# Optimization experiments

Hardware: AMD Instinct MI355X
Metric: run time of the kernel (lower is better)

## Reference

```python
import jax, jax.numpy as jnp
import numpy as np

HEADS = 16
DIM_HEAD = 64
SCALE = DIM_HEAD ** -0.5
LN_EPS = 1e-5


def setup_inputs() -> dict:
    key = jax.random.key(0)
    k1, k2, k3 = jax.random.split(key, 3)
    b, s, d = 2, 2048, 1024
    inner = HEADS * DIM_HEAD
    x = jax.random.normal(k1, (b, s, d), dtype=jnp.float32)
    w_qkv = jax.random.normal(k2, (d, 3 * inner), dtype=jnp.float32) * (d ** -0.5)
    w_out = jax.random.normal(k3, (inner, d), dtype=jnp.float32) * (inner ** -0.5)
    return {
        "x": x,
        "ln_gamma": jnp.ones((d,), jnp.float32),
        "ln_beta": jnp.zeros((d,), jnp.float32),
        "w_qkv": w_qkv,
        "w_out": w_out,
        "b_out": jnp.zeros((d,), jnp.float32),
    }


def _layernorm(x, gamma, beta):
    mu = jnp.mean(x, axis=-1, keepdims=True)
    var = jnp.var(x, axis=-1, keepdims=True)
    return (x - mu) * jax.lax.rsqrt(var + LN_EPS) * gamma + beta


def reference(x, ln_gamma, ln_beta, w_qkv, w_out, b_out):
    b, s, d = x.shape
    xn = _layernorm(x, ln_gamma, ln_beta)
    qkv = xn @ w_qkv                       # [b, s, 3*inner]
    q, k, v = jnp.split(qkv, 3, axis=-1)
    def heads(t):
        return t.reshape(b, s, HEADS, DIM_HEAD).transpose(0, 2, 1, 3)  # [b, h, s, dh]
    q, k, v = heads(q), heads(k), heads(v)
    dots = jnp.einsum("bhqd,bhkd->bhqk", q, k) * SCALE   # [b, h, s, s]
    attn = jax.nn.softmax(dots, axis=-1)
    out = jnp.einsum("bhqk,bhkd->bhqd", attn, v)          # [b, h, s, dh]
    out = out.transpose(0, 2, 1, 3).reshape(b, s, HEADS * DIM_HEAD)
    return out @ w_out + b_out
```

## Files before the change

### kernel.cpp

```cpp
#include <hip/hip_runtime.h>
#include <hip/hip_bf16.h>
#include <stdint.h>

#define NH     16
#define DHEAD  64
#define SEQ    2048
#define DMODEL 1024
#define NBATCH 2
#define INNER  1024
#define QKVN   3072
#define ROWS   4096
#define ATT_QB 128
#define ATT_KB 64
#define KSPLIT 2

typedef __attribute__((ext_vector_type(8))) __bf16 bf16x8;
typedef __attribute__((ext_vector_type(4))) float floatx4;

__device__ __forceinline__ unsigned short f2bf(float f) {
    union { __bf16 b; unsigned short u; } c; c.b = (__bf16)f; return c.u;
}

typedef __attribute__((address_space(1))) void gvoid;
typedef __attribute__((address_space(3))) void lvoid;
__device__ __forceinline__ void gl_lds16(const void* g, void* l) {
    __builtin_amdgcn_global_load_lds((gvoid*)g, (lvoid*)l, 16, 0, 0);
}

__global__ __launch_bounds__(256) void transpose_f2b(
        const float* __restrict__ in, unsigned short* __restrict__ out,
        int rows, int cols) {
    __shared__ unsigned short tile[32][33];
    const int bx = blockIdx.x * 32, by = blockIdx.y * 32;
    const int tx = threadIdx.x & 31, ty = threadIdx.x >> 5;
    for (int i = ty; i < 32; i += 8)
        tile[i][tx] = f2bf(in[(size_t)(by + i) * cols + bx + tx]);
    __syncthreads();
    for (int i = ty; i < 32; i += 8)
        out[(size_t)(bx + i) * rows + by + tx] = tile[tx][i];
}

__global__ __launch_bounds__(256) void ln_kernel(
        const float* __restrict__ x,
        const float* __restrict__ gamma,
        const float* __restrict__ beta,
        unsigned short* __restrict__ xn) {
    __shared__ float red[4][2];
    const int row = blockIdx.x, t = threadIdx.x;
    const size_t base = (size_t)row * DMODEL + t * 4;
    float4 v = *(const float4*)(x + base);
    float s  = v.x + v.y + v.z + v.w;
    float ss = v.x*v.x + v.y*v.y + v.z*v.z + v.w*v.w;
    for (int off = 32; off >= 1; off >>= 1) {
        s  += __shfl_xor(s,  off);
        ss += __shfl_xor(ss, off);
    }
    const int w = t >> 6, lane = t & 63;
    if (lane == 0) { red[w][0] = s; red[w][1] = ss; }
    __syncthreads();
    if (t == 0) {
        float S  = red[0][0] + red[1][0] + red[2][0] + red[3][0];
        float SS = red[0][1] + red[1][1] + red[2][1] + red[3][1];
        float mu  = S * (1.f / DMODEL);
        float var = SS * (1.f / DMODEL) - mu * mu;
        red[0][0] = mu; red[0][1] = rsqrtf(var + 1e-5f);
    }
    __syncthreads();
    const float mu = red[0][0], rstd = red[0][1];
    float4 g = *(const float4*)(gamma + t * 4);
    float4 bb = *(const float4*)(beta + t * 4);
    ushort4 o;
    o.x = f2bf((v.x - mu) * rstd * g.x + bb.x);
    o.y = f2bf((v.y - mu) * rstd * g.y + bb.y);
    o.z = f2bf((v.z - mu) * rstd * g.z + bb.z);
    o.w = f2bf((v.w - mu) * rstd * g.w + bb.w);
    *(ushort4*)(xn + base) = o;
}

__global__ __launch_bounds__(256) void gemm_qkv(
        const unsigned short* __restrict__ A,
        const unsigned short* __restrict__ Bt,
        unsigned short* __restrict__ qP,
        unsigned short* __restrict__ kP,
        unsigned short* __restrict__ vT) {
    const int K = DMODEL;
    __shared__ __align__(16) unsigned short sA[128 * 32];
    __shared__ __align__(16) unsigned short sB[128 * 32];
    __shared__ __align__(16) unsigned short tb[2][64 * 72];
    const int t = threadIdx.x;
    const int mBase = blockIdx.y * 128, nBase = blockIdx.x * 128;
    const int w = t >> 6, lane = t & 63, quad = lane >> 4, l16 = lane & 15;
    const int wm = (w >> 1) * 64, wn = (w & 1) * 64;
    const int srow = t >> 2, sch = t & 3;
    floatx4 acc[4][4];
    for (int mi = 0; mi < 4; mi++)
        for (int ni = 0; ni < 4; ni++) acc[mi][ni] = (floatx4)0.f;

    for (int k0 = 0; k0 < K; k0 += 32) {
        #pragma unroll
        for (int c = 0; c < 2; c++) {
            const int row = c * 64 + srow;
            const int gcol = (sch ^ ((row >> 1) & 3)) * 8;
            gl_lds16(&A[(size_t)(mBase + row) * K + k0 + gcol], &sA[(c * 256 + w * 64) * 8]);
            gl_lds16(&Bt[(size_t)(nBase + row) * K + k0 + gcol], &sB[(c * 256 + w * 64) * 8]);
        }
        __syncthreads();
        bf16x8 af[4], bfv[4];
        #pragma unroll
        for (int mi = 0; mi < 4; mi++) {
            const int r = wm + mi * 16 + l16;
            af[mi] = *(const bf16x8*)&sA[r * 32 + (quad ^ ((r >> 1) & 3)) * 8];
        }
        #pragma unroll
        for (int ni = 0; ni < 4; ni++) {
            const int r = wn + ni * 16 + l16;
            bfv[ni] = *(const bf16x8*)&sB[r * 32 + (quad ^ ((r >> 1) & 3)) * 8];
        }
        #pragma unroll
        for (int mi = 0; mi < 4; mi++)
            #pragma unroll
            for (int ni = 0; ni < 4; ni++)
                acc[mi][ni] = __builtin_amdgcn_mfma_f32_16x16x32_bf16(
                    af[mi], bfv[ni], acc[mi][ni], 0, 0, 0);
        __syncthreads();
    }
    const int reg = nBase >> 10;
    if (reg == 2) {
        #pragma unroll
        for (int ni = 0; ni < 4; ni++) {
            const int col = nBase + wn + ni * 16 + l16;
            const int h = (col & 1023) >> 6, dh = col & 63;
            #pragma unroll
            for (int mi = 0; mi < 4; mi++) {
                const int row0 = mBase + wm + mi * 16 + quad * 4;
                const int b = row0 >> 11, s0 = row0 & 2047;
                ushort4 o;
                o.x = f2bf(acc[mi][ni][0]); o.y = f2bf(acc[mi][ni][1]);
                o.z = f2bf(acc[mi][ni][2]); o.w = f2bf(acc[mi][ni][3]);
                *(ushort4*)&vT[((size_t)(b * NH + h) * DHEAD + dh) * SEQ + s0] = o;
            }
        }
    } else {
        unsigned short* dst = (reg == 0) ? qP : kP;
        const float scl = (reg == 0) ? 0.125f : 1.f;
        const int hh = ((nBase + wn) & 1023) >> 6;
        #pragma unroll
        for (int ph = 0; ph < 2; ph++) {
            if ((w >> 1) == ph) {
                unsigned short* tb_ = &tb[w & 1][0];
                #pragma unroll
                for (int mi = 0; mi < 4; mi++)
                    #pragma unroll
                    for (int ni = 0; ni < 4; ni++)
                        #pragma unroll
                        for (int i = 0; i < 4; i++)
                            tb_[(mi * 16 + quad * 4 + i) * 72 + ni * 16 + l16] =
                                f2bf(acc[mi][ni][i] * scl);
                asm volatile("s_waitcnt lgkmcnt(0)" ::: "memory");
                const int row_g = mBase + wm + lane;
                const int b = row_g >> 11, sr = row_g & 2047;
                unsigned short* orow = dst + ((size_t)(b * NH + hh) * SEQ + sr) * DHEAD;
                #pragma unroll
                for (int c = 0; c < 8; c++)
                    *(bf16x8*)&orow[c * 8] = *(const bf16x8*)&tb_[lane * 72 + c * 8];
            }
            __syncthreads();
        }
    }
}

__global__ __launch_bounds__(256) void gemm_out(
        const unsigned short* __restrict__ A,
        const unsigned short* __restrict__ Bt,
        float* __restrict__ C,
        const int M, const int N, const int K,
        const float* __restrict__ bias) {
    __shared__ __align__(16) unsigned short sA[128 * 32];
    __shared__ __align__(16) unsigned short sB[64 * 32];
    const int t = threadIdx.x;
    const int mBase = blockIdx.y * 128, nBase = blockIdx.x * 64;
    const int w = t >> 6, lane = t & 63, quad = lane >> 4, l16 = lane & 15;
    const int wm = (w >> 1) * 64, wn = (w & 1) * 32;
    const int srow = t >> 2, sch = t & 3;
    floatx4 acc[4][2];
    for (int mi = 0; mi < 4; mi++)
        for (int ni = 0; ni < 2; ni++) acc[mi][ni] = (floatx4)0.f;

    for (int k0 = 0; k0 < K; k0 += 32) {
        #pragma unroll
        for (int c = 0; c < 2; c++) {
            const int row = c * 64 + srow;
            const int gcol = (sch ^ ((row >> 1) & 3)) * 8;
            gl_lds16(&A[(size_t)(mBase + row) * K + k0 + gcol], &sA[(c * 256 + w * 64) * 8]);
        }
        {
            const int gcol = (sch ^ ((srow >> 1) & 3)) * 8;
            gl_lds16(&Bt[(size_t)(nBase + srow) * K + k0 + gcol], &sB[(w * 64) * 8]);
        }
        __syncthreads();
        bf16x8 af[4], bfv[2];
        #pragma unroll
        for (int mi = 0; mi < 4; mi++) {
            const int r = wm + mi * 16 + l16;
            af[mi] = *(const bf16x8*)&sA[r * 32 + (quad ^ ((r >> 1) & 3)) * 8];
        }
        #pragma unroll
        for (int ni = 0; ni < 2; ni++) {
            const int r = wn + ni * 16 + l16;
            bfv[ni] = *(const bf16x8*)&sB[r * 32 + (quad ^ ((r >> 1) & 3)) * 8];
        }
        #pragma unroll
        for (int mi = 0; mi < 4; mi++)
            #pragma unroll
            for (int ni = 0; ni < 2; ni++)
                acc[mi][ni] = __builtin_amdgcn_mfma_f32_16x16x32_bf16(
                    af[mi], bfv[ni], acc[mi][ni], 0, 0, 0);
        __syncthreads();
    }
    #pragma unroll
    for (int mi = 0; mi < 4; mi++)
        #pragma unroll
        for (int ni = 0; ni < 2; ni++) {
            const int col = nBase + wn + ni * 16 + l16;
            const float badd = bias ? bias[col] : 0.f;
            #pragma unroll
            for (int i = 0; i < 4; i++) {
                const int row = mBase + wm + mi * 16 + quad * 4 + i;
                C[(size_t)row * N + col] = acc[mi][ni][i] + badd;
            }
        }
}

__global__ __launch_bounds__(256) void attn_kernel(
        const unsigned short* __restrict__ qP,
        const unsigned short* __restrict__ kP,
        const unsigned short* __restrict__ vT,
        float* __restrict__ Opart,
        float* __restrict__ lpart) {
    __shared__ __align__(16) unsigned short sK[2][ATT_KB * 64];
    __shared__ __align__(16) unsigned short sV[2][ATT_KB * 64];
    __shared__ __align__(16) unsigned short sP[4][2][16 * 64];
    const int t = threadIdx.x, w = t >> 6, lane = t & 63;
    const int quad = lane >> 4, l16 = lane & 15;
    const int bh = blockIdx.y, b = bh >> 4, h = bh & 15;
    const int z = blockIdx.z;
    const int kvBase = z * (SEQ / KSPLIT);
    const int qbase = blockIdx.x * ATT_QB + w * 32;
    const int swr = l16 & 7;

    bf16x8 aq[2][2];
    #pragma unroll
    for (int st = 0; st < 2; st++)
        #pragma unroll
        for (int hh = 0; hh < 2; hh++)
            aq[st][hh] = *(const bf16x8*)&qP[
                ((size_t)bh * SEQ + qbase + st * 16 + l16) * DHEAD + hh * 32 + quad * 8];

    floatx4 oac[2][4];
    float lS[2] = {0.f, 0.f};
    #pragma unroll
    for (int st = 0; st < 2; st++)
        #pragma unroll
        for (int c = 0; c < 4; c++) oac[st][c] = (floatx4)0.f;

    const unsigned short* kb = kP + (size_t)bh * SEQ * DHEAD;
    const unsigned short* vb = vT + (size_t)bh * DHEAD * SEQ;
    const int r8 = lane >> 3, sw8 = ((lane & 7) ^ r8) * 8;

    auto stage = [&](int it, int bi) {
        const int kv0 = kvBase + it * ATT_KB;
        #pragma unroll
        for (int ii = 0; ii < 2; ii++) {
            const int row = w * 16 + ii * 8 + r8;
            gl_lds16(kb + (size_t)(kv0 + row) * DHEAD + sw8,
                     (void*)&sK[bi][(w * 16 + ii * 8) * 64]);
            gl_lds16(vb + (size_t)row * SEQ + kv0 + sw8,
                     (void*)&sV[bi][(w * 16 + ii * 8) * 64]);
        }
    };
    stage(0, 0);

    const int NIT = SEQ / KSPLIT / ATT_KB;
    for (int it = 0; it < NIT; ++it) {
        __syncthreads();
        if (it + 1 < NIT) stage(it + 1, (it + 1) & 1);
        const unsigned short* sKb = &sK[it & 1][0];
        const unsigned short* sVb = &sV[it & 1][0];

        bf16x8 kf[4][2];
        #pragma unroll
        for (int c = 0; c < 4; c++)
            #pragma unroll
            for (int hh = 0; hh < 2; hh++)
                kf[c][hh] = *(const bf16x8*)&sKb[(c * 16 + l16) * 64 +
                                                 8 * (((hh << 2) | quad) ^ swr)];
        floatx4 sv[2][4];
        #pragma unroll
        for (int st = 0; st < 2; st++)
            #pragma unroll
            for (int c = 0; c < 4; c++) {
                floatx4 a = (floatx4)0.f;
                a = __builtin_amdgcn_mfma_f32_16x16x32_bf16(kf[c][0], aq[st][0], a, 0, 0, 0);
                a = __builtin_amdgcn_mfma_f32_16x16x32_bf16(kf[c][1], aq[st][1], a, 0, 0, 0);
                sv[st][c] = a;
            }
        #pragma unroll
        for (int st = 0; st < 2; st++) {
            float sum = 0.f;
            unsigned short* pb = (unsigned short*)&sP[w][st][0];
            #pragma unroll
            for (int c = 0; c < 4; c++) {
                float p0 = __expf(sv[st][c][0]), p1 = __expf(sv[st][c][1]);
                float p2 = __expf(sv[st][c][2]), p3 = __expf(sv[st][c][3]);
                sum += (p0 + p1) + (p2 + p3);
                ushort4 pk;
                pk.x = f2bf(p0); pk.y = f2bf(p1); pk.z = f2bf(p2); pk.w = f2bf(p3);
                *(ushort4*)&pb[l16 * 64 + 8 * ((((c << 1) | (quad >> 1))) ^ swr) + (quad & 1) * 4] = pk;
            }
            sum += __shfl_xor(sum, 16);
            sum += __shfl_xor(sum, 32);
            lS[st] += sum;
        }
        bf16x8 vf[4][2];
        #pragma unroll
        for (int c = 0; c < 4; c++)
            #pragma unroll
            for (int hh = 0; hh < 2; hh++)
                vf[c][hh] = *(const bf16x8*)&sVb[(c * 16 + l16) * 64 +
                                                 8 * (((hh << 2) | quad) ^ swr)];
        asm volatile("s_waitcnt lgkmcnt(0)" ::: "memory");
        #pragma unroll
        for (int st = 0; st < 2; st++) {
            const unsigned short* pb = (const unsigned short*)&sP[w][st][0];
            bf16x8 pf[2];
            #pragma unroll
            for (int hh = 0; hh < 2; hh++)
                pf[hh] = *(const bf16x8*)&pb[l16 * 64 + 8 * (((hh << 2) | quad) ^ swr)];
            #pragma unroll
            for (int c = 0; c < 4; c++) {
                oac[st][c] = __builtin_amdgcn_mfma_f32_16x16x32_bf16(vf[c][0], pf[0], oac[st][c], 0, 0, 0);
                oac[st][c] = __builtin_amdgcn_mfma_f32_16x16x32_bf16(vf[c][1], pf[1], oac[st][c], 0, 0, 0);
            }
        }
    }
    float* Ob = Opart + (size_t)z * ROWS * INNER;
    #pragma unroll
    for (int st = 0; st < 2; st++) {
        const size_t rb = (size_t)(b * SEQ + qbase + st * 16 + l16) * INNER + h * DHEAD;
        #pragma unroll
        for (int c = 0; c < 4; c++) {
            float4 o;
            o.x = oac[st][c][0]; o.y = oac[st][c][1];
            o.z = oac[st][c][2]; o.w = oac[st][c][3];
            *(float4*)&Ob[rb + c * 16 + quad * 4] = o;
        }
    }
    if (quad == 0) {
        #pragma unroll
        for (int st = 0; st < 2; st++)
            lpart[((size_t)z * NBATCH * NH + bh) * SEQ + qbase + st * 16 + l16] = lS[st];
    }
}

__global__ __launch_bounds__(256) void attn_combine(
        const float* __restrict__ Opart,
        const float* __restrict__ lpart,
        unsigned short* __restrict__ aout) {
    const int row = blockIdx.x, t = threadIdx.x;
    const int b = row >> 11, s = row & 2047;
    __shared__ float rls[16];
    if (t < 16) {
        const size_t i0 = ((size_t)(b * NH + t)) * SEQ + s;
        rls[t] = 1.f / (lpart[i0] + lpart[(size_t)NBATCH * NH * SEQ + i0]);
    }
    __syncthreads();
    const size_t base = (size_t)row * INNER + t * 4;
    float4 o0 = *(const float4*)(Opart + base);
    float4 o1 = *(const float4*)(Opart + (size_t)ROWS * INNER + base);
    const float rl = rls[t >> 4];
    ushort4 o;
    o.x = f2bf((o0.x + o1.x) * rl);
    o.y = f2bf((o0.y + o1.y) * rl);
    o.z = f2bf((o0.z + o1.z) * rl);
    o.w = f2bf((o0.w + o1.w) * rl);
    *(ushort4*)&aout[base] = o;
}

extern "C" void kernel_launch(void* const* d_in, const int* in_sizes, int n_in,
                              void* d_out, int out_size, void* d_ws, size_t ws_size,
                              hipStream_t stream) {
    const float* x     = (const float*)d_in[0];
    const float* gamma = (const float*)d_in[1];
    const float* beta  = (const float*)d_in[2];
    const float* wqkv  = (const float*)d_in[3];
    const float* wout  = (const float*)d_in[4];
    const float* bout  = (const float*)d_in[5];
    float* out = (float*)d_out;

    unsigned short* ws     = (unsigned short*)d_ws;
    unsigned short* xn     = ws;
    unsigned short* wqkvT  = xn     + (size_t)ROWS * DMODEL;
    unsigned short* qPb    = wqkvT  + (size_t)QKVN * DMODEL;
    unsigned short* kPb    = qPb    + (size_t)NBATCH * NH * SEQ * DHEAD;
    unsigned short* vTb    = kPb    + (size_t)NBATCH * NH * SEQ * DHEAD;
    unsigned short* attnO  = vTb    + (size_t)NBATCH * NH * SEQ * DHEAD;
    unsigned short* woutT  = attnO  + (size_t)ROWS * INNER;
    float* Opart = (float*)(woutT + (size_t)DMODEL * INNER);
    float* lpart = Opart + (size_t)KSPLIT * ROWS * INNER;

    transpose_f2b<<<dim3(QKVN / 32, DMODEL / 32), 256, 0, stream>>>(wqkv, wqkvT, DMODEL, QKVN);
    transpose_f2b<<<dim3(DMODEL / 32, INNER / 32), 256, 0, stream>>>(wout, woutT, INNER, DMODEL);
    ln_kernel<<<ROWS, 256, 0, stream>>>(x, gamma, beta, xn);
    gemm_qkv<<<dim3(QKVN / 128, ROWS / 128), 256, 0, stream>>>(xn, wqkvT, qPb, kPb, vTb);
    attn_kernel<<<dim3(SEQ / ATT_QB, NBATCH * NH, KSPLIT), 256, 0, stream>>>(
        qPb, kPb, vTb, Opart, lpart);
    attn_combine<<<ROWS, 256, 0, stream>>>(Opart, lpart, attnO);
    gemm_out<<<dim3(DMODEL / 64, ROWS / 128), 256, 0, stream>>>(
        attnO, woutT, out, ROWS, DMODEL, INNER, bout);
}
```

Baseline: 226.3 us.

## Merge prep kernels, enlarge out-GEMM tile, shrink attention P buffer

Merges the layernorm and the two weight transpose/cast kernels into a single launch that branches on block index, removing two kernel launches. Widens the output GEMM tile from 128x64 to 128x128, which halves its grid and raises per-block reuse of A. In attention, sets a minimum occupancy hint, hoists the V fragment loads ahead of the softmax, and reuses a single per-wave P buffer per sub-tile to cut LDS use. The larger GEMM tile leaves only 256 blocks, which may underfill the GPU, and the occupancy hint may cause register spills.

```diff
diff --git a/kernel.cpp b/kernel.cpp
--- a/kernel.cpp
+++ b/kernel.cpp
@@ -27,54 +27,66 @@
     __builtin_amdgcn_global_load_lds((gvoid*)g, (lvoid*)l, 16, 0, 0);
 }
 
-__global__ __launch_bounds__(256) void transpose_f2b(
-        const float* __restrict__ in, unsigned short* __restrict__ out,
-        int rows, int cols) {
-    __shared__ unsigned short tile[32][33];
-    const int bx = blockIdx.x * 32, by = blockIdx.y * 32;
-    const int tx = threadIdx.x & 31, ty = threadIdx.x >> 5;
-    for (int i = ty; i < 32; i += 8)
-        tile[i][tx] = f2bf(in[(size_t)(by + i) * cols + bx + tx]);
-    __syncthreads();
-    for (int i = ty; i < 32; i += 8)
-        out[(size_t)(bx + i) * rows + by + tx] = tile[tx][i];
-}
-
-__global__ __launch_bounds__(256) void ln_kernel(
+__global__ __launch_bounds__(256) void prep_kernel(
         const float* __restrict__ x,
         const float* __restrict__ gamma,
         const float* __restrict__ beta,
-        unsigned short* __restrict__ xn) {
+        const float* __restrict__ wqkv,
+        const float* __restrict__ wout,
+        unsigned short* __restrict__ xn,
+        unsigned short* __restrict__ wqkvT,
+        unsigned short* __restrict__ woutT) {
+    __shared__ unsigned short tile[32][33];
     __shared__ float red[4][2];
-    const int row = blockIdx.x, t = threadIdx.x;
-    const size_t base = (size_t)row * DMODEL + t * 4;
-    float4 v = *(const float4*)(x + base);
-    float s  = v.x + v.y + v.z + v.w;
-    float ss = v.x*v.x + v.y*v.y + v.z*v.z + v.w*v.w;
-    for (int off = 32; off >= 1; off >>= 1) {
-        s  += __shfl_xor(s,  off);
-        ss += __shfl_xor(ss, off);
-    }
-    const int w = t >> 6, lane = t & 63;
-    if (lane == 0) { red[w][0] = s; red[w][1] = ss; }
-    __syncthreads();
-    if (t == 0) {
-        float S  = red[0][0] + red[1][0] + red[2][0] + red[3][0];
-        float SS = red[0][1] + red[1][1] + red[2][1] + red[3][1];
-        float mu  = S * (1.f / DMODEL);
-        float var = SS * (1.f / DMODEL) - mu * mu;
-        red[0][0] = mu; red[0][1] = rsqrtf(var + 1e-5f);
-    }
-    __syncthreads();
-    const float mu = red[0][0], rstd = red[0][1];
-    float4 g = *(const float4*)(gamma + t * 4);
-    float4 bb = *(const float4*)(beta + t * 4);
-    ushort4 o;
-    o.x = f2bf((v.x - mu) * rstd * g.x + bb.x);
-    o.y = f2bf((v.y - mu) * rstd * g.y + bb.y);
-    o.z = f2bf((v.z - mu) * rstd * g.z + bb.z);
-    o.w = f2bf((v.w - mu) * rstd * g.w + bb.w);
-    *(ushort4*)(xn + base) = o;
+    const int bid = blockIdx.x, t = threadIdx.x;
+    if (bid < ROWS) {
+        const size_t base = (size_t)bid * DMODEL + t * 4;
+        float4 v = *(const float4*)(x + base);
+        float s  = v.x + v.y + v.z + v.w;
+        float ss = v.x*v.x + v.y*v.y + v.z*v.z + v.w*v.w;
+        for (int off = 32; off >= 1; off >>= 1) {
+            s  += __shfl_xor(s,  off);
+            ss += __shfl_xor(ss, off);
+        }
+        const int w = t >> 6, lane = t & 63;
+        if (lane == 0) { red[w][0] = s; red[w][1] = ss; }
+        __syncthreads();
+        if (t == 0) {
+            float S  = red[0][0] + red[1][0] + red[2][0] + red[3][0];
+            float SS = red[0][1] + red[1][1] + red[2][1] + red[3][1];
+            float mu  = S * (1.f / DMODEL);
+            float var = SS * (1.f / DMODEL) - mu * mu;
+            red[0][0] = mu; red[0][1] = rsqrtf(var + 1e-5f);
+        }
+        __syncthreads();
+        const float mu = red[0][0], rstd = red[0][1];
+        float4 g = *(const float4*)(gamma + t * 4);
+        float4 bb = *(const float4*)(beta + t * 4);
+        ushort4 o;
+        o.x = f2bf((v.x - mu) * rstd * g.x + bb.x);
+        o.y = f2bf((v.y - mu) * rstd * g.y + bb.y);
+        o.z = f2bf((v.z - mu) * rstd * g.z + bb.z);
+        o.w = f2bf((v.w - mu) * rstd * g.w + bb.w);
+        *(ushort4*)(xn + base) = o;
+    } else if (bid < ROWS + (QKVN / 32) * (DMODEL / 32)) {
+        const int tid = bid - ROWS;
+        const int bx = (tid % (QKVN / 32)) * 32, by = (tid / (QKVN / 32)) * 32;
+        const int tx = t & 31, ty = t >> 5;
+        for (int i = ty; i < 32; i += 8)
+            tile[i][tx] = f2bf(wqkv[(size_t)(by + i) * QKVN + bx + tx]);
+        __syncthreads();
+        for (int i = ty; i < 32; i += 8)
+            wqkvT[(size_t)(bx + i) * DMODEL + by + tx] = tile[tx][i];
+    } else {
+        const int tid = bid - ROWS - (QKVN / 32) * (DMODEL / 32);
+        const int bx = (tid & 31) * 32, by = (tid >> 5) * 32;
+        const int tx = t & 31, ty = t >> 5;
+        for (int i = ty; i < 32; i += 8)
+            tile[i][tx] = f2bf(wout[(size_t)(by + i) * DMODEL + bx + tx]);
+        __syncthreads();
+        for (int i = ty; i < 32; i += 8)
+            woutT[(size_t)(bx + i) * INNER + by + tx] = tile[tx][i];
+    }
 }
 
 __global__ __launch_bounds__(256) void gemm_qkv(
@@ -169,69 +181,7 @@
     }
 }
 
-__global__ __launch_bounds__(256) void gemm_out(
-        const unsigned short* __restrict__ A,
-        const unsigned short* __restrict__ Bt,
-        float* __restrict__ C,
-        const int M, const int N, const int K,
-        const float* __restrict__ bias) {
-    __shared__ __align__(16) unsigned short sA[128 * 32];
-    __shared__ __align__(16) unsigned short sB[64 * 32];
-    const int t = threadIdx.x;
-    const int mBase = blockIdx.y * 128, nBase = blockIdx.x * 64;
-    const int w = t >> 6, lane = t & 63, quad = lane >> 4, l16 = lane & 15;
-    const int wm = (w >> 1) * 64, wn = (w & 1) * 32;
-    const int srow = t >> 2, sch = t & 3;
-    floatx4 acc[4][2];
-    for (int mi = 0; mi < 4; mi++)
-        for (int ni = 0; ni < 2; ni++) acc[mi][ni] = (floatx4)0.f;
-
-    for (int k0 = 0; k0 < K; k0 += 32) {
-        #pragma unroll
-        for (int c = 0; c < 2; c++) {
-            const int row = c * 64 + srow;
-            const int gcol = (sch ^ ((row >> 1) & 3)) * 8;
-            gl_lds16(&A[(size_t)(mBase + row) * K + k0 + gcol], &sA[(c * 256 + w * 64) * 8]);
-        }
-        {
-            const int gcol = (sch ^ ((srow >> 1) & 3)) * 8;
-            gl_lds16(&Bt[(size_t)(nBase + srow) * K + k0 + gcol], &sB[(w * 64) * 8]);
-        }
-        __syncthreads();
-        bf16x8 af[4], bfv[2];
-        #pragma unroll
-        for (int mi = 0; mi < 4; mi++) {
-            const int r = wm + mi * 16 + l16;
-            af[mi] = *(const bf16x8*)&sA[r * 32 + (quad ^ ((r >> 1) & 3)) * 8];
-        }
-        #pragma unroll
-        for (int ni = 0; ni < 2; ni++) {
-            const int r = wn + ni * 16 + l16;
-            bfv[ni] = *(const bf16x8*)&sB[r * 32 + (quad ^ ((r >> 1) & 3)) * 8];
-        }
-        #pragma unroll
-        for (int mi = 0; mi < 4; mi++)
-            #pragma unroll
-            for (int ni = 0; ni < 2; ni++)
-                acc[mi][ni] = __builtin_amdgcn_mfma_f32_16x16x32_bf16(
-                    af[mi], bfv[ni], acc[mi][ni], 0, 0, 0);
-        __syncthreads();
-    }
-    #pragma unroll
-    for (int mi = 0; mi < 4; mi++)
-        #pragma unroll
-        for (int ni = 0; ni < 2; ni++) {
-            const int col = nBase + wn + ni * 16 + l16;
-            const float badd = bias ? bias[col] : 0.f;
-            #pragma unroll
-            for (int i = 0; i < 4; i++) {
-                const int row = mBase + wm + mi * 16 + quad * 4 + i;
-                C[(size_t)row * N + col] = acc[mi][ni][i] + badd;
-            }
-        }
-}
-
-__global__ __launch_bounds__(256) void attn_kernel(
+__global__ __launch_bounds__(256, 4) void attn_kernel(
         const unsigned short* __restrict__ qP,
         const unsigned short* __restrict__ kP,
         const unsigned short* __restrict__ vT,
@@ -239,7 +189,7 @@
         float* __restrict__ lpart) {
     __shared__ __align__(16) unsigned short sK[2][ATT_KB * 64];
     __shared__ __align__(16) unsigned short sV[2][ATT_KB * 64];
-    __shared__ __align__(16) unsigned short sP[4][2][16 * 64];
+    __shared__ __align__(16) unsigned short sP[4][16 * 64];
     const int t = threadIdx.x, w = t >> 6, lane = t & 63;
     const int quad = lane >> 4, l16 = lane & 15;
     const int bh = blockIdx.y, b = bh >> 4, h = bh & 15;
@@ -304,10 +254,17 @@
                 a = __builtin_amdgcn_mfma_f32_16x16x32_bf16(kf[c][1], aq[st][1], a, 0, 0, 0);
                 sv[st][c] = a;
             }
+        bf16x8 vf[4][2];
+        #pragma unroll
+        for (int c = 0; c < 4; c++)
+            #pragma unroll
+            for (int hh = 0; hh < 2; hh++)
+                vf[c][hh] = *(const bf16x8*)&sVb[(c * 16 + l16) * 64 +
+                                                 8 * (((hh << 2) | quad) ^ swr)];
+        unsigned short* pb = (unsigned short*)&sP[w][0];
         #pragma unroll
         for (int st = 0; st < 2; st++) {
             float sum = 0.f;
-            unsigned short* pb = (unsigned short*)&sP[w][st][0];
             #pragma unroll
             for (int c = 0; c < 4; c++) {
                 float p0 = __expf(sv[st][c][0]), p1 = __expf(sv[st][c][1]);
@@ -320,18 +277,7 @@
             sum += __shfl_xor(sum, 16);
             sum += __shfl_xor(sum, 32);
             lS[st] += sum;
-        }
-        bf16x8 vf[4][2];
-        #pragma unroll
-        for (int c = 0; c < 4; c++)
-            #pragma unroll
-            for (int hh = 0; hh < 2; hh++)
-                vf[c][hh] = *(const bf16x8*)&sVb[(c * 16 + l16) * 64 +
-                                                 8 * (((hh << 2) | quad) ^ swr)];
-        asm volatile("s_waitcnt lgkmcnt(0)" ::: "memory");
-        #pragma unroll
-        for (int st = 0; st < 2; st++) {
-            const unsigned short* pb = (const unsigned short*)&sP[w][st][0];
+            asm volatile("s_waitcnt lgkmcnt(0)" ::: "memory");
             bf16x8 pf[2];
             #pragma unroll
             for (int hh = 0; hh < 2; hh++)
@@ -386,6 +332,65 @@
     *(ushort4*)&aout[base] = o;
 }
 
+__global__ __launch_bounds__(256) void gemm_out(
+        const unsigned short* __restrict__ A,
+        const unsigned short* __restrict__ Bt,
+        float* __restrict__ C,
+        const int M, const int N, const int K,
+        const float* __restrict__ bias) {
+    __shared__ __align__(16) unsigned short sA[128 * 32];
+    __shared__ __align__(16) unsigned short sB[128 * 32];
+    const int t = threadIdx.x;
+    const int mBase = blockIdx.y * 128, nBase = blockIdx.x * 128;
+    const int w = t >> 6, lane = t & 63, quad = lane >> 4, l16 = lane & 15;
+    const int wm = (w >> 1) * 64, wn = (w & 1) * 64;
+    const int srow = t >> 2, sch = t & 3;
+    floatx4 acc[4][4];
+    for (int mi = 0; mi < 4; mi++)
+        for (int ni = 0; ni < 4; ni++) acc[mi][ni] = (floatx4)0.f;
+
+    for (int k0 = 0; k0 < K; k0 += 32) {
+        #pragma unroll
+        for (int c = 0; c < 2; c++) {
+            const int row = c * 64 + srow;
+            const int gcol = (sch ^ ((row >> 1) & 3)) * 8;
+            gl_lds16(&A[(size_t)(mBase + row) * K + k0 + gcol], &sA[(c * 256 + w * 64) * 8]);
+            gl_lds16(&Bt[(size_t)(nBase + row) * K + k0 + gcol], &sB[(c * 256 + w * 64) * 8]);
+        }
+        __syncthreads();
+        bf16x8 af[4], bfv[4];
+        #pragma unroll
+        for (int mi = 0; mi < 4; mi++) {
+            const int r = wm + mi * 16 + l16;
+            af[mi] = *(const bf16x8*)&sA[r * 32 + (quad ^ ((r >> 1) & 3)) * 8];
+        }
+        #pragma unroll
+        for (int ni = 0; ni < 4; ni++) {
+            const int r = wn + ni * 16 + l16;
+            bfv[ni] = *(const bf16x8*)&sB[r * 32 + (quad ^ ((r >> 1) & 3)) * 8];
+        }
+        #pragma unroll
+        for (int mi = 0; mi < 4; mi++)
+            #pragma unroll
+            for (int ni = 0; ni < 4; ni++)
+                acc[mi][ni] = __builtin_amdgcn_mfma_f32_16x16x32_bf16(
+                    af[mi], bfv[ni], acc[mi][ni], 0, 0, 0);
+        __syncthreads();
+    }
+    #pragma unroll
+    for (int mi = 0; mi < 4; mi++)
+        #pragma unroll
+        for (int ni = 0; ni < 4; ni++) {
+            const int col = nBase + wn + ni * 16 + l16;
+            const float badd = bias ? bias[col] : 0.f;
+            #pragma unroll
+            for (int i = 0; i < 4; i++) {
+                const int row = mBase + wm + mi * 16 + quad * 4 + i;
+                C[(size_t)row * N + col] = acc[mi][ni][i] + badd;
+            }
+        }
+}
+
 extern "C" void kernel_launch(void* const* d_in, const int* in_sizes, int n_in,
                               void* d_out, int out_size, void* d_ws, size_t ws_size,
                               hipStream_t stream) {
@@ -408,13 +413,12 @@
     float* Opart = (float*)(woutT + (size_t)DMODEL * INNER);
     float* lpart = Opart + (size_t)KSPLIT * ROWS * INNER;
 
-    transpose_f2b<<<dim3(QKVN / 32, DMODEL / 32), 256, 0, stream>>>(wqkv, wqkvT, DMODEL, QKVN);
-    transpose_f2b<<<dim3(DMODEL / 32, INNER / 32), 256, 0, stream>>>(wout, woutT, INNER, DMODEL);
-    ln_kernel<<<ROWS, 256, 0, stream>>>(x, gamma, beta, xn);
+    const int PREP_BLKS = ROWS + (QKVN / 32) * (DMODEL / 32) + (DMODEL / 32) * (INNER / 32);
+    prep_kernel<<<PREP_BLKS, 256, 0, stream>>>(x, gamma, beta, wqkv, wout, xn, wqkvT, woutT);
     gemm_qkv<<<dim3(QKVN / 128, ROWS / 128), 256, 0, stream>>>(xn, wqkvT, qPb, kPb, vTb);
     attn_kernel<<<dim3(SEQ / ATT_QB, NBATCH * NH, KSPLIT), 256, 0, stream>>>(
         qPb, kPb, vTb, Opart, lpart);
     attn_combine<<<ROWS, 256, 0, stream>>>(Opart, lpart, attnO);
-    gemm_out<<<dim3(DMODEL / 64, ROWS / 128), 256, 0, stream>>>(
+    gemm_out<<<dim3(DMODEL / 128, ROWS / 128), 256, 0, stream>>>(
         attnO, woutT, out, ROWS, DMODEL, INNER, bout);
 }
```

New measurement: 274.1 us. 1.21x slower.
